# Kernel optimization log

Measured on AMD Instinct MI355X. Metric: run time of the kernel, lower is better.

Reference implementation:

```python
import jax, jax.numpy as jnp
import numpy as np

DIM = 512
HEADS = 8
DHEAD = 64
WIN = 128
QK_SCALE = 8.0
LN_EPS = 1e-5


def setup_inputs() -> dict:
    key = jax.random.key(0)
    ks = jax.random.split(key, 5)
    B, N = 8, 4096
    x = jax.random.normal(ks[0], (B, N, DIM), jnp.float32)
    w_qkv = jax.random.normal(ks[1], (3 * HEADS * DHEAD, DIM), jnp.float32) * 0.02
    w_out = jax.random.normal(ks[2], (DIM, HEADS * DHEAD), jnp.float32) * 0.02
    b_out = jnp.zeros((DIM,), jnp.float32)
    w_ff1 = jax.random.normal(ks[3], (4 * DIM, DIM), jnp.float32) * 0.02
    w_ff2 = jax.random.normal(ks[4], (DIM, 4 * DIM), jnp.float32) * 0.02
    return {
        'x': x, 'w_qkv': w_qkv,
        'q_scale': jnp.ones((DHEAD,), jnp.float32),
        'k_scale': jnp.ones((DHEAD,), jnp.float32),
        'w_out': w_out, 'b_out': b_out,
        'ln1_g': jnp.ones((DIM,), jnp.float32), 'ln1_b': jnp.zeros((DIM,), jnp.float32),
        'ff_ln_g': jnp.ones((DIM,), jnp.float32), 'ff_ln_b': jnp.zeros((DIM,), jnp.float32),
        'w_ff1': w_ff1, 'w_ff2': w_ff2,
    }


def _ln(x, g, b):
    m = jnp.mean(x, axis=-1, keepdims=True)
    v = jnp.mean((x - m) ** 2, axis=-1, keepdims=True)
    return (x - m) * jax.lax.rsqrt(v + LN_EPS) * g + b


def _l2norm(t):
    return t / jnp.clip(jnp.linalg.norm(t, axis=-1, keepdims=True), 1e-12)


def _rotary(t, pos):
    # t: (B, H, N, DHEAD); standard (non-xpos) rotary, half-split style
    inv_freq = 1.0 / (10000.0 ** (jnp.arange(0, DHEAD, 2, dtype=jnp.float32) / DHEAD))
    freqs = pos[:, None] * inv_freq                      # (N, DHEAD/2)
    emb = jnp.concatenate([freqs, freqs], axis=-1)       # (N, DHEAD)
    cos, sin = jnp.cos(emb), jnp.sin(emb)
    t1, t2 = t[..., : DHEAD // 2], t[..., DHEAD // 2:]
    rot = jnp.concatenate([-t2, t1], axis=-1)
    return t * cos + rot * sin


def reference(x, w_qkv, q_scale, k_scale, w_out, b_out, ln1_g, ln1_b,
              ff_ln_g, ff_ln_b, w_ff1, w_ff2):
    B, N, D = x.shape
    nw = N // WIN

    # ---- LocalMHA (prenorm, qk-rmsnorm, sliding window, causal) ----
    h = _ln(x, ln1_g, ln1_b)
    qkv = h @ w_qkv.T                                    # (B, N, 3*H*DHEAD)
    q, k, v = jnp.split(qkv, 3, axis=-1)

    def to_heads(t):
        return t.reshape(B, N, HEADS, DHEAD).transpose(0, 2, 1, 3)  # (B,H,N,d)

    q, k, v = to_heads(q), to_heads(k), to_heads(v)
    q = _l2norm(q) * q_scale
    k = _l2norm(k) * k_scale
    pos = jnp.arange(N, dtype=jnp.float32)
    q = _rotary(q, pos)
    k = _rotary(k, pos)

    # bucket into windows; keys/values look back one window
    bq = q.reshape(B, HEADS, nw, WIN, DHEAD)
    bk = k.reshape(B, HEADS, nw, WIN, DHEAD)
    bv = v.reshape(B, HEADS, nw, WIN, DHEAD)

    def look_back(t):
        prev = jnp.concatenate([jnp.zeros_like(t[:, :, :1]), t[:, :, :-1]], axis=2)
        return jnp.concatenate([prev, t], axis=3)

    kk, vv = look_back(bk), look_back(bv)

    qpos = jnp.arange(N, dtype=jnp.int32).reshape(nw, WIN)
    kprev = jnp.concatenate([jnp.full((1, WIN), -1, jnp.int32), qpos[:-1]], axis=0)
    kpos = jnp.concatenate([kprev, qpos], axis=1)
    mask = (qpos[:, :, None] >= kpos[:, None, :]) & (kpos[:, None, :] >= 0)

    sim = jnp.einsum('bhnid,bhnjd->bhnij', bq, kk) * QK_SCALE
    sim = jnp.where(mask, sim, -1e9)
    attn = jax.nn.softmax(sim, axis=-1)
    out = jnp.einsum('bhnij,bhnjd->bhnid', attn, vv)
    out = out.reshape(B, HEADS, N, DHEAD).transpose(0, 2, 1, 3).reshape(B, N, HEADS * DHEAD)
    x = x + out @ w_out.T + b_out

    # ---- FeedForward: LN -> Linear(4D, no bias) -> GELU -> Linear(D, no bias) ----
    hf = _ln(x, ff_ln_g, ff_ln_b)
    ff = jax.nn.gelu(hf @ w_ff1.T, approximate=False) @ w_ff2.T
    return x + ff
```

## Files before the change

kernel.cpp:

```cpp
#include <hip/hip_runtime.h>
#include <cstdint>
#include <cstddef>

typedef __bf16 bf16;
typedef __bf16 bf16x8 __attribute__((ext_vector_type(8)));
typedef float f32x4 __attribute__((ext_vector_type(4)));

#define DEV static __device__ __forceinline__

constexpr int BATCH = 8;
constexpr int SEQ = 4096;
constexpr int DIM = 512;
constexpr int HEADS = 8;
constexpr int DH = 64;
constexpr int WIN = 128;
constexpr int NW = SEQ / WIN;
constexpr int TOK = BATCH * SEQ;
constexpr float EPS = 1e-5f;

constexpr size_t R_EL   = (size_t)TOK * DIM;
constexpr size_t C_QKV  = 0;
constexpr size_t C_WOUT = 786432;
constexpr size_t C_WF1  = 1048576;
constexpr size_t C_WF2  = 2097152;
constexpr size_t C_SM   = 3145728;
constexpr size_t P_EL   = 3148416;

DEV void gload_lds16(const void* g, void* l) {
  __builtin_amdgcn_global_load_lds((__attribute__((address_space(1))) void*)g,
                                   (__attribute__((address_space(3))) void*)l,
                                   16, 0, 0);
}

DEV f32x4 mfma16(bf16x8 a, bf16x8 b, f32x4 c) {
  return __builtin_amdgcn_mfma_f32_16x16x32_bf16(a, b, c, 0, 0, 0);
}

DEV float fast_gelu(float v) {
  const float z = fabsf(v) * 0.7071067811865476f;
  const float t = __builtin_amdgcn_rcpf(1.0f + 0.3275911f * z);
  const float p = t * (0.254829592f +
                  t * (-0.284496736f +
                  t * (1.421413741f +
                  t * (-1.453152027f +
                  t * 1.061405429f))));
  const float e = __expf(-z * z);
  const float erfa = 1.0f - p * e;
  const float cdf = 0.5f + copysignf(0.5f * erfa, v);
  return v * cdf;
}

struct SrcPtrs { const void* p[12]; };

DEV void copy8(const void* src, long si, bf16* dst, bool f32) {
  if (f32) {
    const float4* s = (const float4*)((const float*)src + si);
    float4 a = s[0], b = s[1];
    bf16x8 o;
    o[0] = (bf16)a.x; o[1] = (bf16)a.y; o[2] = (bf16)a.z; o[3] = (bf16)a.w;
    o[4] = (bf16)b.x; o[5] = (bf16)b.y; o[6] = (bf16)b.z; o[7] = (bf16)b.w;
    *(bf16x8*)dst = o;
  } else {
    *(bf16x8*)dst = *(const bf16x8*)((const bf16*)src + si);
  }
}

__global__ __launch_bounds__(256) void ingest_kernel(SrcPtrs sp, bf16* cano) {
  const bool f32 = (((const unsigned short*)sp.p[2])[0] == 0);
  const long e = (long)threadIdx.x * 8;
  int b = blockIdx.x;
  if (b < 384)  { long o = (long)b * 2048 + e; copy8(sp.p[1], o, cano + C_QKV + o, f32); return; }
  b -= 384;
  if (b < 128)  { long o = (long)b * 2048 + e; copy8(sp.p[4], o, cano + C_WOUT + o, f32); return; }
  b -= 128;
  if (b < 512)  { long o = (long)b * 2048 + e; copy8(sp.p[10], o, cano + C_WF1 + o, f32); return; }
  b -= 512;
  if (b < 512)  { long o = (long)b * 2048 + e; copy8(sp.p[11], o, cano + C_WF2 + o, f32); return; }
  b -= 512;
  const long o = (long)b * 2048 + e;
  if (o >= 2688) return;
  const void* src; long si;
  if      (o < 64)   { src = sp.p[2]; si = o; }
  else if (o < 128)  { src = sp.p[3]; si = o - 64; }
  else if (o < 640)  { src = sp.p[5]; si = o - 128; }
  else if (o < 1152) { src = sp.p[6]; si = o - 640; }
  else if (o < 1664) { src = sp.p[7]; si = o - 1152; }
  else if (o < 2176) { src = sp.p[8]; si = o - 1664; }
  else               { src = sp.p[9]; si = o - 2176; }
  copy8(src, si, cano + C_SM + o, f32);
}

__global__ __launch_bounds__(256) void ln_kernel(const void* __restrict__ in,
                                                 const bf16* __restrict__ gg,
                                                 const bf16* __restrict__ bb,
                                                 bf16* __restrict__ out,
                                                 const unsigned short* __restrict__ probe,
                                                 int raw) {
  const int wave = threadIdx.x >> 6, lane = threadIdx.x & 63;
  const int row = blockIdx.x * 4 + wave;
  const size_t base = (size_t)row * DIM + lane * 8;
  float f[8];
  if (raw && probe[0] == 0) {
    const float4* p = (const float4*)((const float*)in + base);
    float4 a = p[0], bq = p[1];
    f[0] = a.x; f[1] = a.y; f[2] = a.z; f[3] = a.w;
    f[4] = bq.x; f[5] = bq.y; f[6] = bq.z; f[7] = bq.w;
  } else {
    bf16x8 v = *(const bf16x8*)((const bf16*)in + base);
#pragma unroll
    for (int i = 0; i < 8; ++i) f[i] = (float)v[i];
  }
  float s = 0.f, sq = 0.f;
#pragma unroll
  for (int i = 0; i < 8; ++i) { s += f[i]; sq += f[i] * f[i]; }
#pragma unroll
  for (int m = 32; m; m >>= 1) { s += __shfl_xor(s, m); sq += __shfl_xor(sq, m); }
  const float mean = s * (1.0f / DIM);
  const float var = fmaxf(sq * (1.0f / DIM) - mean * mean, 0.0f);
  const float rs = rsqrtf(var + EPS);
  bf16x8 gv = *(const bf16x8*)(gg + lane * 8);
  bf16x8 bv = *(const bf16x8*)(bb + lane * 8);
  bf16x8 o;
#pragma unroll
  for (int i = 0; i < 8; ++i) o[i] = (bf16)((f[i] - mean) * rs * (float)gv[i] + (float)bv[i]);
  *(bf16x8*)((bf16*)out + base) = o;
}

template <int MODE>
__global__ __launch_bounds__(256) void gemm_bt(const bf16* __restrict__ A,
                                               const bf16* __restrict__ Bw,
                                               bf16* __restrict__ O0, bf16* __restrict__ O1,
                                               bf16* __restrict__ O2,
                                               float* __restrict__ Of,
                                               const void* __restrict__ Xraw,
                                               const bf16* __restrict__ Xb,
                                               const bf16* __restrict__ bias,
                                               const unsigned short* __restrict__ probe,
                                               int K, int bstride, int ostride, int gx) {
  __shared__ __align__(16) bf16 smem[4 * 128 * 32];
  const int tid = threadIdx.x;
  const int wave = tid >> 6, lane = tid & 63;
  const int l15 = lane & 15, quad = lane >> 4;
  const int id = blockIdx.x;
  const int per = gx * 8;
  const int tM = ((id / per) * 8 + (id & 7)) * 128;
  const int tN = ((id % per) >> 3) * 128;
  const int wM = (wave >> 1) * 64, wN = (wave & 1) * 64;
  f32x4 acc[4][4];
  const f32x4 z = {0.f, 0.f, 0.f, 0.f};
#pragma unroll
  for (int i = 0; i < 4; ++i)
#pragma unroll
    for (int j = 0; j < 4; ++j) acc[i][j] = z;

  auto stage = [&](int k0, int p) {
    bf16* dA = smem + p * 8192;
    bf16* dB = dA + 4096;
#pragma unroll
    for (int t = 0; t < 2; ++t) {
      const int c = tid + t * 256;
      const int row = c >> 2, cc = (c & 3) * 8;
      gload_lds16(A + (size_t)(tM + row) * K + k0 + cc, &dA[c * 8]);
      gload_lds16(Bw + (size_t)(tN + row) * bstride + k0 + cc, &dB[c * 8]);
    }
  };

  stage(0, 0);
  int cur = 0;
  for (int k0 = 0; k0 < K; k0 += 32) {
    __syncthreads();
    if (k0 + 32 < K) stage(k0 + 32, cur ^ 1);
    const bf16* As = smem + cur * 8192;
    const bf16* Bs = As + 4096;
    bf16x8 aF[4], bF[4];
#pragma unroll
    for (int i = 0; i < 4; ++i) aF[i] = *(const bf16x8*)&As[(wM + i * 16 + l15) * 32 + quad * 8];
#pragma unroll
    for (int j = 0; j < 4; ++j) bF[j] = *(const bf16x8*)&Bs[(wN + j * 16 + l15) * 32 + quad * 8];
#pragma unroll
    for (int i = 0; i < 4; ++i)
#pragma unroll
      for (int j = 0; j < 4; ++j) acc[i][j] = mfma16(aF[i], bF[j], acc[i][j]);
    cur ^= 1;
  }

  if constexpr (MODE == 0) {
    __syncthreads();
    bf16* ob = smem + wave * 1152;
    const int colbase = tN + wN;
    const int which = colbase >> 9;
    const int head = (colbase >> 6) & 7;
    bf16* dst = which == 0 ? O0 : (which == 1 ? O1 : O2);
    const int ch = lane & 7;
    float scv[8], invf[8];
    if (which < 2) {
      const bf16* sc = which ? bias : Xb;
      bf16x8 s8 = *(const bf16x8*)(sc + ch * 8);
#pragma unroll
      for (int u = 0; u < 8; ++u) {
        scv[u] = (float)s8[u] * (which == 0 ? 8.0f : 1.0f);
        invf[u] = exp2f(-(float)((ch & 3) * 8 + u) * (13.287712379549449f / 32.0f));
      }
    }
#pragma unroll
    for (int i = 0; i < 4; ++i) {
#pragma unroll
      for (int j = 0; j < 4; ++j)
#pragma unroll
        for (int r = 0; r < 4; ++r)
          ob[(quad * 4 + r) * 72 + j * 16 + l15] = (bf16)acc[i][j][r];
#pragma unroll
      for (int t = 0; t < 2; ++t) {
        const int rr = t * 8 + (lane >> 3);
        const int rowg = tM + wM + i * 16 + rr;
        bf16x8 ov = *(const bf16x8*)&ob[rr * 72 + ch * 8];
        float f[8];
#pragma unroll
        for (int u = 0; u < 8; ++u) f[u] = (float)ov[u];
        if (which < 2) {
          float ss = 0.f;
#pragma unroll
          for (int u = 0; u < 8; ++u) ss += f[u] * f[u];
          ss += __shfl_xor(ss, 1); ss += __shfl_xor(ss, 2); ss += __shfl_xor(ss, 4);
          const float rs = 1.0f / fmaxf(sqrtf(ss), 1e-12f);
#pragma unroll
          for (int u = 0; u < 8; ++u) f[u] *= rs * scv[u];
          float pf[8];
#pragma unroll
          for (int u = 0; u < 8; ++u) pf[u] = __shfl_xor(f[u], 4);
          const float pos = (float)(rowg & (SEQ - 1));
#pragma unroll
          for (int u = 0; u < 8; ++u) {
            float sn, cs;
            __sincosf(pos * invf[u], &sn, &cs);
            const float rot = (ch < 4) ? -pf[u] : pf[u];
            f[u] = f[u] * cs + rot * sn;
          }
        }
        bf16x8 o8;
#pragma unroll
        for (int u = 0; u < 8; ++u) o8[u] = (bf16)f[u];
        const int bb = rowg >> 12, n = rowg & (SEQ - 1);
        *(bf16x8*)(dst + ((size_t)(bb * HEADS + head) * SEQ + n) * DH + ch * 8) = o8;
      }
    }
    return;
  }

  if constexpr (MODE == 1 || MODE == 2) {
    __syncthreads();
    bf16* ob = smem + wave * 1152;
    const int ch = lane & 7;
    bf16x8 bias8;
    bool xf32 = false;
    if constexpr (MODE == 1) {
      bias8 = *(const bf16x8*)(bias + tN + wN + ch * 8);
      xf32 = (probe[0] == 0);
    }
#pragma unroll
    for (int i = 0; i < 4; ++i) {
#pragma unroll
      for (int j = 0; j < 4; ++j)
#pragma unroll
        for (int r = 0; r < 4; ++r)
          ob[(quad * 4 + r) * 72 + j * 16 + l15] = (bf16)acc[i][j][r];
#pragma unroll
      for (int t = 0; t < 2; ++t) {
        const int rr = t * 8 + (lane >> 3);
        const int rowg = tM + wM + i * 16 + rr;
        bf16x8 ov = *(const bf16x8*)&ob[rr * 72 + ch * 8];
        bf16x8 o8;
        if constexpr (MODE == 1) {
          const size_t idx = (size_t)rowg * DIM + tN + wN + ch * 8;
          float xr[8];
          if (xf32) {
            const float4* xp = (const float4*)((const float*)Xraw + idx);
            float4 a = xp[0], bq = xp[1];
            xr[0] = a.x; xr[1] = a.y; xr[2] = a.z; xr[3] = a.w;
            xr[4] = bq.x; xr[5] = bq.y; xr[6] = bq.z; xr[7] = bq.w;
          } else {
            bf16x8 xv = *(const bf16x8*)((const bf16*)Xraw + idx);
#pragma unroll
            for (int u = 0; u < 8; ++u) xr[u] = (float)xv[u];
          }
#pragma unroll
          for (int u = 0; u < 8; ++u) o8[u] = (bf16)((float)ov[u] + xr[u] + (float)bias8[u]);
          *(bf16x8*)(O0 + idx) = o8;
        } else {
#pragma unroll
          for (int u = 0; u < 8; ++u) {
            o8[u] = (bf16)fast_gelu((float)ov[u]);
          }
          *(bf16x8*)(O0 + (size_t)rowg * ostride + tN + wN + ch * 8) = o8;
        }
      }
    }
    return;
  }

  if constexpr (MODE == 3 || MODE == 4) {
    __syncthreads();
    float* obf = (float*)smem + wave * 1088;
    const int ch = lane & 7;
#pragma unroll
    for (int i = 0; i < 4; ++i) {
#pragma unroll
      for (int j = 0; j < 4; ++j)
#pragma unroll
        for (int r = 0; r < 4; ++r)
          obf[(quad * 4 + r) * 68 + j * 16 + l15] = acc[i][j][r];
#pragma unroll
      for (int t = 0; t < 2; ++t) {
        const int rr = t * 8 + (lane >> 3);
        const int rowg = tM + wM + i * 16 + rr;
        const size_t idx = (size_t)rowg * DIM + tN + wN + ch * 8;
        const float4* rp = (const float4*)&obf[rr * 68 + ch * 8];
        float4 a = rp[0], b = rp[1];
        float f[8] = {a.x, a.y, a.z, a.w, b.x, b.y, b.z, b.w};
        if constexpr (MODE == 3) {
          bf16x8 xv = *(const bf16x8*)(Xb + idx);
#pragma unroll
          for (int u = 0; u < 8; ++u) f[u] += (float)xv[u];
        } else {
          const float4* op = (const float4*)(Of + idx);
          float4 oa = op[0], ob4 = op[1];
          f[0] += oa.x; f[1] += oa.y; f[2] += oa.z; f[3] += oa.w;
          f[4] += ob4.x; f[5] += ob4.y; f[6] += ob4.z; f[7] += ob4.w;
        }
        float4 o0 = {f[0], f[1], f[2], f[3]}, o1 = {f[4], f[5], f[6], f[7]};
        ((float4*)(Of + idx))[0] = o0;
        ((float4*)(Of + idx))[1] = o1;
      }
    }
    return;
  }
}

__global__ __launch_bounds__(256, 3) void attn_kernel(const bf16* __restrict__ q,
                                                      const bf16* __restrict__ k,
                                                      const bf16* __restrict__ v,
                                                      bf16* __restrict__ ao) {
  __shared__ __align__(16) bf16 kv[256 * 72];
  __shared__ __align__(16) bf16 pbuf[4][16 * 136];
  const int w = blockIdx.x, h = blockIdx.y, b = blockIdx.z;
  const int tid = threadIdx.x;
  const int wv = tid >> 6, lane = tid & 63;
  const int l15 = lane & 15, quad = lane >> 4;
  const size_t bh = (size_t)b * HEADS + h;
  const bf16* qb = q + bh * SEQ * DH;
  const bf16* kb = k + bh * SEQ * DH;
  const bf16* vb = v + bh * SEQ * DH;
  const int t0 = (w - 1) * WIN;

#pragma unroll
  for (int it = 0; it < 8; ++it) {
    const int c = it * 256 + tid;
    const int tok = c >> 3, ch = c & 7;
    int gt = t0 + tok; gt = gt < 0 ? 0 : gt;
    *(bf16x8*)&kv[tok * 72 + ch * 8] = *(const bf16x8*)(kb + (size_t)gt * DH + ch * 8);
  }
  bf16x8 aQ[2][2];
#pragma unroll
  for (int qt = 0; qt < 2; ++qt) {
    const int qtok = w * WIN + wv * 32 + qt * 16 + l15;
#pragma unroll
    for (int ks = 0; ks < 2; ++ks)
      aQ[qt][ks] = *(const bf16x8*)(qb + (size_t)qtok * DH + ks * 32 + quad * 8);
  }
  int gtv = t0 + tid; gtv = gtv < 0 ? 0 : gtv;
  bf16x8 vld[8];
#pragma unroll
  for (int dg = 0; dg < 8; ++dg)
    vld[dg] = *(const bf16x8*)(vb + (size_t)gtv * DH + dg * 8);
  __syncthreads();

  bf16x8 aP[2][8];
#pragma unroll
  for (int qt = 0; qt < 2; ++qt) {
    f32x4 sreg[16];
#pragma unroll
    for (int nt = 0; nt < 16; ++nt) {
      f32x4 a = {0.f, 0.f, 0.f, 0.f};
#pragma unroll
      for (int ks = 0; ks < 2; ++ks) {
        bf16x8 bK = *(const bf16x8*)&kv[(nt * 16 + l15) * 72 + ks * 32 + quad * 8];
        a = mfma16(aQ[qt][ks], bK, a);
      }
      sreg[nt] = a;
    }
    const int qlb = wv * 32 + qt * 16 + quad * 4;
    float rinv[4];
#pragma unroll
    for (int r = 0; r < 4; ++r) {
      const int ql = qlb + r;
      float sum = 0.f;
#pragma unroll
      for (int nt = 0; nt < 16; ++nt) {
        const int j = nt * 16 + l15;
        const bool valid = (nt < 8) ? (w > 0) : (ql >= j - WIN);
        const float p = valid ? __expf(sreg[nt][r]) : 0.0f;
        sreg[nt][r] = p;
        sum += p;
      }
#pragma unroll
      for (int m = 8; m; m >>= 1) sum += __shfl_xor(sum, m);
      rinv[r] = 1.0f / sum;
    }
#pragma unroll
    for (int half = 0; half < 2; ++half) {
#pragma unroll
      for (int ntw = 0; ntw < 8; ++ntw)
#pragma unroll
        for (int r = 0; r < 4; ++r)
          pbuf[wv][(quad * 4 + r) * 136 + ntw * 16 + l15] =
              (bf16)(sreg[half * 8 + ntw][r] * rinv[r]);
#pragma unroll
      for (int kk = 0; kk < 4; ++kk)
        aP[qt][half * 4 + kk] = *(const bf16x8*)&pbuf[wv][l15 * 136 + kk * 32 + quad * 8];
    }
  }
  __syncthreads();

#pragma unroll
  for (int dg = 0; dg < 8; ++dg)
#pragma unroll
    for (int i = 0; i < 8; ++i)
      kv[(dg * 8 + i) * 264 + tid] = vld[dg][i];
  __syncthreads();

#pragma unroll
  for (int qt = 0; qt < 2; ++qt) {
#pragma unroll
    for (int dt = 0; dt < 4; ++dt) {
      f32x4 o = {0.f, 0.f, 0.f, 0.f};
#pragma unroll
      for (int ks2 = 0; ks2 < 8; ++ks2) {
        bf16x8 bV = *(const bf16x8*)&kv[(dt * 16 + l15) * 264 + ks2 * 32 + quad * 8];
        o = mfma16(aP[qt][ks2], bV, o);
      }
#pragma unroll
      for (int r = 0; r < 4; ++r)
        pbuf[wv][(quad * 4 + r) * 136 + dt * 16 + l15] = (bf16)o[r];
    }
#pragma unroll
    for (int t = 0; t < 2; ++t) {
      const int rr = t * 8 + (lane >> 3), ch = lane & 7;
      bf16x8 ov = *(const bf16x8*)&pbuf[wv][rr * 136 + ch * 8];
      const int tok = w * WIN + wv * 32 + qt * 16 + rr;
      *(bf16x8*)(ao + ((size_t)b * SEQ + tok) * DIM + h * DH + ch * 8) = ov;
    }
  }
}

extern "C" void kernel_launch(void* const* d_in, const int* in_sizes, int n_in,
                              void* d_out, int out_size, void* d_ws, size_t ws_size,
                              hipStream_t stream) {
  (void)in_sizes; (void)n_in; (void)out_size;
  float* out = (float*)d_out;
  bf16* cano = (bf16*)d_ws;
  const unsigned short* probe = (const unsigned short*)d_in[2];

  SrcPtrs sp;
  for (int i = 0; i < 12; ++i) sp.p[i] = d_in[i];

  bf16* slot0 = cano + P_EL;
  bf16* slot1 = cano + P_EL + R_EL;
  bf16* slot2 = cano + P_EL + 2 * R_EL;
  bf16* slot3 = cano + P_EL + 3 * R_EL;

  const bf16* qsc  = cano + C_SM + 0;
  const bf16* ksc  = cano + C_SM + 64;
  const bf16* bout = cano + C_SM + 128;
  const bf16* l1g  = cano + C_SM + 640;
  const bf16* l1b  = cano + C_SM + 1152;
  const bf16* lfg  = cano + C_SM + 1664;
  const bf16* lfb  = cano + C_SM + 2176;

  ingest_kernel<<<1538, 256, 0, stream>>>(sp, cano);
  ln_kernel<<<TOK / 4, 256, 0, stream>>>(d_in[0], l1g, l1b, slot0, probe, 1);
  gemm_bt<0><<<12 * 256, 256, 0, stream>>>(slot0, cano + C_QKV, slot1, slot2, slot3,
                                           nullptr, nullptr, qsc, ksc, probe,
                                           DIM, DIM, 0, 12);
  attn_kernel<<<dim3(NW, HEADS, BATCH), 256, 0, stream>>>(slot1, slot2, slot3, slot0);
  gemm_bt<1><<<4 * 256, 256, 0, stream>>>(slot0, cano + C_WOUT, slot1, nullptr, nullptr,
                                          nullptr, d_in[0], nullptr, bout, probe,
                                          DIM, DIM, 0, 4);
  ln_kernel<<<TOK / 4, 256, 0, stream>>>(slot1, lfg, lfb, slot0, probe, 0);

  const bool big = ws_size >= (size_t)(P_EL + 6 * R_EL) * 2;
  if (big) {
    bf16* f1 = slot2;
    gemm_bt<2><<<16 * 256, 256, 0, stream>>>(slot0, cano + C_WF1, f1, nullptr, nullptr,
                                             nullptr, nullptr, nullptr, nullptr, probe,
                                             DIM, DIM, 2048, 16);
    gemm_bt<3><<<4 * 256, 256, 0, stream>>>(f1, cano + C_WF2, nullptr, nullptr, nullptr,
                                            out, nullptr, slot1, nullptr, probe,
                                            2048, 2048, 0, 4);
  } else {
    bf16* f1h = slot2;
    for (int half = 0; half < 2; ++half) {
      const bf16* w1h = cano + C_WF1 + (size_t)half * 1024 * DIM;
      const bf16* w2h = cano + C_WF2 + (size_t)half * 1024;
      gemm_bt<2><<<8 * 256, 256, 0, stream>>>(slot0, w1h, f1h, nullptr, nullptr,
                                              nullptr, nullptr, nullptr, nullptr, probe,
                                              DIM, DIM, 1024, 8);
      if (half == 0)
        gemm_bt<3><<<4 * 256, 256, 0, stream>>>(f1h, w2h, nullptr, nullptr, nullptr,
                                                out, nullptr, slot1, nullptr, probe,
                                                1024, 2048, 0, 4);
      else
        gemm_bt<4><<<4 * 256, 256, 0, stream>>>(f1h, w2h, nullptr, nullptr, nullptr,
                                                out, nullptr, nullptr, nullptr, probe,
                                                1024, 2048, 0, 4);
    }
  }
}
```

Baseline: 508.0 us.

## Replace GEMM with 256x256-tile 8-wave kernel using swizzled LDS and interleaved prefetch

Replaces the 128x128, 4-wave, 32-deep-K GEMM with a 256x256 tile, 8-wave (512-thread) kernel using 64-deep K steps, XOR-swizzled LDS layout and 128KB dynamic shared memory. Global-to-LDS loads for later K tiles are interleaved between MFMA quarter blocks, with explicit barriers, waitcnt and setprio to overlap memory with compute. The aim is more data reuse per tile and better load/compute overlap. In exchange it uses more registers, more LDS and fewer blocks, which lowers occupancy and tail balance on the smaller GEMMs.

```diff
diff --git a/kernel.cpp b/kernel.cpp
--- a/kernel.cpp
+++ b/kernel.cpp
@@ -126,68 +126,135 @@
   *(bf16x8*)((bf16*)out + base) = o;
 }
 
+
+#define SYNC_PRE \
+  __builtin_amdgcn_sched_barrier(0); \
+  __builtin_amdgcn_s_barrier(); \
+  asm volatile("s_waitcnt lgkmcnt(0)" ::: "memory"); \
+  __builtin_amdgcn_sched_barrier(0); \
+  __builtin_amdgcn_s_setprio(1);
+
+#define SYNC_POST \
+  __builtin_amdgcn_s_setprio(0); \
+  __builtin_amdgcn_sched_barrier(0); \
+  __builtin_amdgcn_s_barrier();
+
+#define SYNC_POST_VM \
+  __builtin_amdgcn_s_setprio(0); \
+  __builtin_amdgcn_sched_barrier(0); \
+  asm volatile("s_waitcnt vmcnt(4)" ::: "memory"); \
+  __builtin_amdgcn_s_barrier();
+
+#define RD_A4(D, MB) \
+  _Pragma("unroll") for (int mf = 0; mf < 4; ++mf) { \
+    a[mf][0] = *(const bf16x8*)&smem[(D) * 32768 + arow0 + ((MB) + mf) * 1024 + kq0]; \
+    a[mf][1] = *(const bf16x8*)&smem[(D) * 32768 + arow0 + ((MB) + mf) * 1024 + kq1]; \
+  }
+
+#define RD_B2(D, NB, BR) \
+  _Pragma("unroll") for (int nf = 0; nf < 2; ++nf) { \
+    BR[nf][0] = *(const bf16x8*)&smem[(D) * 32768 + brow0 + ((NB) + nf) * 1024 + kq0]; \
+    BR[nf][1] = *(const bf16x8*)&smem[(D) * 32768 + brow0 + ((NB) + nf) * 1024 + kq1]; \
+  }
+
+#define MFMA_Q(MB, NB, BR) \
+  _Pragma("unroll") for (int mf = 0; mf < 4; ++mf) \
+  _Pragma("unroll") for (int nf = 0; nf < 2; ++nf) { \
+    acc[(MB) + mf][(NB) + nf] = mfma16(a[mf][0], BR[nf][0], acc[(MB) + mf][(NB) + nf]); \
+    acc[(MB) + mf][(NB) + nf] = mfma16(a[mf][1], BR[nf][1], acc[(MB) + mf][(NB) + nf]); \
+  }
+
 template <int MODE>
-__global__ __launch_bounds__(256) void gemm_bt(const bf16* __restrict__ A,
-                                               const bf16* __restrict__ Bw,
-                                               bf16* __restrict__ O0, bf16* __restrict__ O1,
-                                               bf16* __restrict__ O2,
-                                               float* __restrict__ Of,
-                                               const void* __restrict__ Xraw,
-                                               const bf16* __restrict__ Xb,
-                                               const bf16* __restrict__ bias,
-                                               const unsigned short* __restrict__ probe,
-                                               int K, int bstride, int ostride, int gx) {
-  __shared__ __align__(16) bf16 smem[4 * 128 * 32];
+__global__ __launch_bounds__(512, 2) void gemm8(const bf16* __restrict__ A,
+                                                const bf16* __restrict__ Bw,
+                                                bf16* __restrict__ O0, bf16* __restrict__ O1,
+                                                bf16* __restrict__ O2,
+                                                float* __restrict__ Of,
+                                                const void* __restrict__ Xraw,
+                                                const bf16* __restrict__ Xb,
+                                                const bf16* __restrict__ bias,
+                                                const unsigned short* __restrict__ probe,
+                                                int K, int bstride, int ostride, int gx) {
+  extern __shared__ __align__(16) bf16 smem[];
   const int tid = threadIdx.x;
-  const int wave = tid >> 6, lane = tid & 63;
+  const int wid = tid >> 6, lane = tid & 63;
   const int l15 = lane & 15, quad = lane >> 4;
+  const int wm = wid >> 2, wn = wid & 3;
   const int id = blockIdx.x;
   const int per = gx * 8;
-  const int tM = ((id / per) * 8 + (id & 7)) * 128;
-  const int tN = ((id % per) >> 3) * 128;
-  const int wM = (wave >> 1) * 64, wN = (wave & 1) * 64;
-  f32x4 acc[4][4];
+  const int tM = ((id / per) * 8 + (id & 7)) * 256;
+  const int tN = ((id % per) >> 3) * 256;
+
+  const int sw = (l15 & 7) << 3;
+  const int kq0 = (quad * 8) ^ sw;
+  const int kq1 = (32 + quad * 8) ^ sw;
+  const int arow0 = (wm * 128 + l15) * 64;
+  const int brow0 = (wn * 64 + l15) * 64 + 16384;
+
+  const int srow = wid * 16 + (lane >> 3);
+  const int scol = ((lane & 7) ^ (lane >> 3)) << 3;
+
+  auto stageA = [&](int d, int h, int T) {
+    const size_t g0 = (size_t)(tM + h * 128 + srow) * K + T * 64 + scol;
+    bf16* dst = smem + d * 32768 + h * 8192 + wid * 1024 + lane * 8;
+#pragma unroll
+    for (int j = 0; j < 2; ++j)
+      gload_lds16(A + g0 + (size_t)j * 8 * K, dst + j * 512);
+  };
+  auto stageB = [&](int d, int h, int T) {
+    const size_t g0 = (size_t)(tN + h * 128 + srow) * bstride + T * 64 + scol;
+    bf16* dst = smem + d * 32768 + 16384 + h * 8192 + wid * 1024 + lane * 8;
+#pragma unroll
+    for (int j = 0; j < 2; ++j)
+      gload_lds16(Bw + g0 + (size_t)j * 8 * bstride, dst + j * 512);
+  };
+
+  f32x4 acc[8][4];
   const f32x4 z = {0.f, 0.f, 0.f, 0.f};
 #pragma unroll
-  for (int i = 0; i < 4; ++i)
+  for (int i = 0; i < 8; ++i)
 #pragma unroll
     for (int j = 0; j < 4; ++j) acc[i][j] = z;
 
-  auto stage = [&](int k0, int p) {
-    bf16* dA = smem + p * 8192;
-    bf16* dB = dA + 4096;
-#pragma unroll
-    for (int t = 0; t < 2; ++t) {
-      const int c = tid + t * 256;
-      const int row = c >> 2, cc = (c & 3) * 8;
-      gload_lds16(A + (size_t)(tM + row) * K + k0 + cc, &dA[c * 8]);
-      gload_lds16(Bw + (size_t)(tN + row) * bstride + k0 + cc, &dB[c * 8]);
-    }
-  };
-
-  stage(0, 0);
-  int cur = 0;
-  for (int k0 = 0; k0 < K; k0 += 32) {
-    __syncthreads();
-    if (k0 + 32 < K) stage(k0 + 32, cur ^ 1);
-    const bf16* As = smem + cur * 8192;
-    const bf16* Bs = As + 4096;
-    bf16x8 aF[4], bF[4];
-#pragma unroll
-    for (int i = 0; i < 4; ++i) aF[i] = *(const bf16x8*)&As[(wM + i * 16 + l15) * 32 + quad * 8];
-#pragma unroll
-    for (int j = 0; j < 4; ++j) bF[j] = *(const bf16x8*)&Bs[(wN + j * 16 + l15) * 32 + quad * 8];
-#pragma unroll
-    for (int i = 0; i < 4; ++i)
-#pragma unroll
-      for (int j = 0; j < 4; ++j) acc[i][j] = mfma16(aF[i], bF[j], acc[i][j]);
-    cur ^= 1;
+  bf16x8 a[4][2], b01[2][2], b23[2][2];
+
+  stageA(0, 0, 0); stageA(0, 1, 0); stageB(0, 0, 0); stageB(0, 1, 0);
+  stageB(1, 0, 1); stageB(1, 1, 1);
+  asm volatile("s_waitcnt vmcnt(4)" ::: "memory");
+  __builtin_amdgcn_s_barrier();
+
+  const int nt = K >> 6;
+  for (int t2 = 0; t2 < nt; t2 += 2) {
+    const int tn2 = (t2 + 2 < nt) ? t2 + 2 : nt - 1;
+    const int tn3 = (t2 + 3 < nt) ? t2 + 3 : nt - 1;
+    RD_A4(0, 0); RD_B2(0, 0, b01);
+    stageA(1, 0, t2 + 1);
+    SYNC_PRE; MFMA_Q(0, 0, b01); SYNC_POST;
+    RD_B2(0, 2, b23);
+    stageA(1, 1, t2 + 1);
+    SYNC_PRE; MFMA_Q(0, 2, b23); SYNC_POST;
+    RD_A4(0, 4);
+    stageB(0, 0, tn2);
+    SYNC_PRE; MFMA_Q(4, 2, b23); SYNC_POST;
+    stageB(0, 1, tn2);
+    SYNC_PRE; MFMA_Q(4, 0, b01); SYNC_POST_VM;
+    RD_A4(1, 0); RD_B2(1, 0, b01);
+    stageA(0, 0, tn2);
+    SYNC_PRE; MFMA_Q(0, 0, b01); SYNC_POST;
+    RD_B2(1, 2, b23);
+    stageA(0, 1, tn2);
+    SYNC_PRE; MFMA_Q(0, 2, b23); SYNC_POST;
+    RD_A4(1, 4);
+    stageB(1, 0, tn3);
+    SYNC_PRE; MFMA_Q(4, 2, b23); SYNC_POST;
+    stageB(1, 1, tn3);
+    SYNC_PRE; MFMA_Q(4, 0, b01); SYNC_POST_VM;
   }
 
   if constexpr (MODE == 0) {
     __syncthreads();
-    bf16* ob = smem + wave * 1152;
-    const int colbase = tN + wN;
+    bf16* ob = smem + wid * 1152;
+    const int colbase = tN + wn * 64;
     const int which = colbase >> 9;
     const int head = (colbase >> 6) & 7;
     bf16* dst = which == 0 ? O0 : (which == 1 ? O1 : O2);
@@ -203,7 +270,7 @@
       }
     }
 #pragma unroll
-    for (int i = 0; i < 4; ++i) {
+    for (int i = 0; i < 8; ++i) {
 #pragma unroll
       for (int j = 0; j < 4; ++j)
 #pragma unroll
@@ -212,7 +279,7 @@
 #pragma unroll
       for (int t = 0; t < 2; ++t) {
         const int rr = t * 8 + (lane >> 3);
-        const int rowg = tM + wM + i * 16 + rr;
+        const int rowg = tM + wm * 128 + i * 16 + rr;
         bf16x8 ov = *(const bf16x8*)&ob[rr * 72 + ch * 8];
         float f[8];
 #pragma unroll
@@ -249,16 +316,16 @@
 
   if constexpr (MODE == 1 || MODE == 2) {
     __syncthreads();
-    bf16* ob = smem + wave * 1152;
+    bf16* ob = smem + wid * 1152;
     const int ch = lane & 7;
     bf16x8 bias8;
     bool xf32 = false;
     if constexpr (MODE == 1) {
-      bias8 = *(const bf16x8*)(bias + tN + wN + ch * 8);
+      bias8 = *(const bf16x8*)(bias + tN + wn * 64 + ch * 8);
       xf32 = (probe[0] == 0);
     }
 #pragma unroll
-    for (int i = 0; i < 4; ++i) {
+    for (int i = 0; i < 8; ++i) {
 #pragma unroll
       for (int j = 0; j < 4; ++j)
 #pragma unroll
@@ -267,16 +334,16 @@
 #pragma unroll
       for (int t = 0; t < 2; ++t) {
         const int rr = t * 8 + (lane >> 3);
-        const int rowg = tM + wM + i * 16 + rr;
+        const int rowg = tM + wm * 128 + i * 16 + rr;
         bf16x8 ov = *(const bf16x8*)&ob[rr * 72 + ch * 8];
         bf16x8 o8;
         if constexpr (MODE == 1) {
-          const size_t idx = (size_t)rowg * DIM + tN + wN + ch * 8;
+          const size_t idx = (size_t)rowg * DIM + tN + wn * 64 + ch * 8;
           float xr[8];
           if (xf32) {
             const float4* xp = (const float4*)((const float*)Xraw + idx);
-            float4 a = xp[0], bq = xp[1];
-            xr[0] = a.x; xr[1] = a.y; xr[2] = a.z; xr[3] = a.w;
+            float4 aa = xp[0], bq = xp[1];
+            xr[0] = aa.x; xr[1] = aa.y; xr[2] = aa.z; xr[3] = aa.w;
             xr[4] = bq.x; xr[5] = bq.y; xr[6] = bq.z; xr[7] = bq.w;
           } else {
             bf16x8 xv = *(const bf16x8*)((const bf16*)Xraw + idx);
@@ -288,10 +355,8 @@
           *(bf16x8*)(O0 + idx) = o8;
         } else {
 #pragma unroll
-          for (int u = 0; u < 8; ++u) {
-            o8[u] = (bf16)fast_gelu((float)ov[u]);
-          }
-          *(bf16x8*)(O0 + (size_t)rowg * ostride + tN + wN + ch * 8) = o8;
+          for (int u = 0; u < 8; ++u) o8[u] = (bf16)fast_gelu((float)ov[u]);
+          *(bf16x8*)(O0 + (size_t)rowg * ostride + tN + wn * 64 + ch * 8) = o8;
         }
       }
     }
@@ -300,10 +365,10 @@
 
   if constexpr (MODE == 3 || MODE == 4) {
     __syncthreads();
-    float* obf = (float*)smem + wave * 1088;
+    float* obf = (float*)smem + wid * 1088;
     const int ch = lane & 7;
 #pragma unroll
-    for (int i = 0; i < 4; ++i) {
+    for (int i = 0; i < 8; ++i) {
 #pragma unroll
       for (int j = 0; j < 4; ++j)
 #pragma unroll
@@ -312,11 +377,11 @@
 #pragma unroll
       for (int t = 0; t < 2; ++t) {
         const int rr = t * 8 + (lane >> 3);
-        const int rowg = tM + wM + i * 16 + rr;
-        const size_t idx = (size_t)rowg * DIM + tN + wN + ch * 8;
+        const int rowg = tM + wm * 128 + i * 16 + rr;
+        const size_t idx = (size_t)rowg * DIM + tN + wn * 64 + ch * 8;
         const float4* rp = (const float4*)&obf[rr * 68 + ch * 8];
-        float4 a = rp[0], b = rp[1];
-        float f[8] = {a.x, a.y, a.z, a.w, b.x, b.y, b.z, b.w};
+        float4 aa = rp[0], bb4 = rp[1];
+        float f[8] = {aa.x, aa.y, aa.z, aa.w, bb4.x, bb4.y, bb4.z, bb4.w};
         if constexpr (MODE == 3) {
           bf16x8 xv = *(const bf16x8*)(Xb + idx);
 #pragma unroll
@@ -476,42 +541,53 @@
   const bf16* lfg  = cano + C_SM + 1664;
   const bf16* lfb  = cano + C_SM + 2176;
 
+  constexpr int LDS8 = 131072;
+  static bool attr_done = false;
+  if (!attr_done) {
+    hipFuncSetAttribute((const void*)gemm8<0>, hipFuncAttributeMaxDynamicSharedMemorySize, LDS8);
+    hipFuncSetAttribute((const void*)gemm8<1>, hipFuncAttributeMaxDynamicSharedMemorySize, LDS8);
+    hipFuncSetAttribute((const void*)gemm8<2>, hipFuncAttributeMaxDynamicSharedMemorySize, LDS8);
+    hipFuncSetAttribute((const void*)gemm8<3>, hipFuncAttributeMaxDynamicSharedMemorySize, LDS8);
+    hipFuncSetAttribute((const void*)gemm8<4>, hipFuncAttributeMaxDynamicSharedMemorySize, LDS8);
+    attr_done = true;
+  }
+
   ingest_kernel<<<1538, 256, 0, stream>>>(sp, cano);
   ln_kernel<<<TOK / 4, 256, 0, stream>>>(d_in[0], l1g, l1b, slot0, probe, 1);
-  gemm_bt<0><<<12 * 256, 256, 0, stream>>>(slot0, cano + C_QKV, slot1, slot2, slot3,
+  gemm8<0><<<128 * 6, 512, LDS8, stream>>>(slot0, cano + C_QKV, slot1, slot2, slot3,
                                            nullptr, nullptr, qsc, ksc, probe,
-                                           DIM, DIM, 0, 12);
+                                           DIM, DIM, 0, 6);
   attn_kernel<<<dim3(NW, HEADS, BATCH), 256, 0, stream>>>(slot1, slot2, slot3, slot0);
-  gemm_bt<1><<<4 * 256, 256, 0, stream>>>(slot0, cano + C_WOUT, slot1, nullptr, nullptr,
-                                          nullptr, d_in[0], nullptr, bout, probe,
-                                          DIM, DIM, 0, 4);
+  gemm8<1><<<128 * 2, 512, LDS8, stream>>>(slot0, cano + C_WOUT, slot1, nullptr, nullptr,
+                                           nullptr, d_in[0], nullptr, bout, probe,
+                                           DIM, DIM, 0, 2);
   ln_kernel<<<TOK / 4, 256, 0, stream>>>(slot1, lfg, lfb, slot0, probe, 0);
 
   const bool big = ws_size >= (size_t)(P_EL + 6 * R_EL) * 2;
   if (big) {
     bf16* f1 = slot2;
-    gemm_bt<2><<<16 * 256, 256, 0, stream>>>(slot0, cano + C_WF1, f1, nullptr, nullptr,
+    gemm8<2><<<128 * 8, 512, LDS8, stream>>>(slot0, cano + C_WF1, f1, nullptr, nullptr,
                                              nullptr, nullptr, nullptr, nullptr, probe,
-                                             DIM, DIM, 2048, 16);
-    gemm_bt<3><<<4 * 256, 256, 0, stream>>>(f1, cano + C_WF2, nullptr, nullptr, nullptr,
-                                            out, nullptr, slot1, nullptr, probe,
-                                            2048, 2048, 0, 4);
+                                             DIM, DIM, 2048, 8);
+    gemm8<3><<<128 * 2, 512, LDS8, stream>>>(f1, cano + C_WF2, nullptr, nullptr, nullptr,
+                                             out, nullptr, slot1, nullptr, probe,
+                                             2048, 2048, 0, 2);
   } else {
     bf16* f1h = slot2;
     for (int half = 0; half < 2; ++half) {
       const bf16* w1h = cano + C_WF1 + (size_t)half * 1024 * DIM;
       const bf16* w2h = cano + C_WF2 + (size_t)half * 1024;
-      gemm_bt<2><<<8 * 256, 256, 0, stream>>>(slot0, w1h, f1h, nullptr, nullptr,
-                                              nullptr, nullptr, nullptr, nullptr, probe,
-                                              DIM, DIM, 1024, 8);
+      gemm8<2><<<128 * 4, 512, LDS8, stream>>>(slot0, w1h, f1h, nullptr, nullptr,
+                                               nullptr, nullptr, nullptr, nullptr, probe,
+                                               DIM, DIM, 1024, 4);
       if (half == 0)
-        gemm_bt<3><<<4 * 256, 256, 0, stream>>>(f1h, w2h, nullptr, nullptr, nullptr,
-                                                out, nullptr, slot1, nullptr, probe,
-                                                1024, 2048, 0, 4);
+        gemm8<3><<<128 * 2, 512, LDS8, stream>>>(f1h, w2h, nullptr, nullptr, nullptr,
+                                                 out, nullptr, slot1, nullptr, probe,
+                                                 1024, 2048, 0, 2);
       else
-        gemm_bt<4><<<4 * 256, 256, 0, stream>>>(f1h, w2h, nullptr, nullptr, nullptr,
-                                                out, nullptr, nullptr, nullptr, probe,
-                                                1024, 2048, 0, 4);
-    }
-  }
-}
+        gemm8<4><<<128 * 2, 512, LDS8, stream>>>(f1h, w2h, nullptr, nullptr, nullptr,
+                                                 out, nullptr, nullptr, nullptr, probe,
+                                                 1024, 2048, 0, 2);
+    }
+  }
+}
```

After: 575.8 us. 1.13x slower.
